# Kernel tuning notes

Measured on AMD Instinct MI355X. Metric: run time of the kernel, lower is better.

## Reference

```python
import jax, jax.numpy as jnp
import numpy as np

L, H, C, HS, E, K, V, BS = 2, 12, 768, 64, 8, 2, 32000, 1024
B, T = 2, 1024


def layer_norm(x, s, b):
    mu = x.mean(-1, keepdims=True)
    var = ((x - mu) ** 2).mean(-1, keepdims=True)
    return (x - mu) / jnp.sqrt(var + 1e-5) * s + b


def setup_inputs() -> dict:
    key = jax.random.key(0)
    ks = jax.random.split(key, 16)
    def n(k, shape, s=0.02):
        return jax.random.normal(k, shape, dtype=jnp.float32) * s
    return {
        'idx': jax.random.randint(ks[0], (B, T), 0, V),
        'targets': jax.random.randint(ks[1], (B, T), 0, V),
        'tok_emb': n(ks[2], (V, C)),
        'pos_emb': n(ks[3], (BS, C)),
        'ln1_s': jnp.ones((L, C), jnp.float32), 'ln1_b': jnp.zeros((L, C), jnp.float32),
        'wq': n(ks[4], (L, H, C, HS)), 'wk': n(ks[5], (L, H, C, HS)), 'wv': n(ks[6], (L, H, C, HS)),
        'wo': n(ks[7], (L, C, C)), 'bo': jnp.zeros((L, C), jnp.float32),
        'ln2_s': jnp.ones((L, C), jnp.float32), 'ln2_b': jnp.zeros((L, C), jnp.float32),
        'gate_w': n(ks[8], (L, E, C)),
        'w1': n(ks[9], (L, E, 4 * C, C)), 'b1': jnp.zeros((L, E, 4 * C), jnp.float32),
        'w2': n(ks[10], (L, E, C, 4 * C)), 'b2': jnp.zeros((L, E, C), jnp.float32),
        'lm_w': n(ks[11], (V, C)), 'lm_b': jnp.zeros((V,), jnp.float32),
    }


def reference(idx, targets, tok_emb, pos_emb, ln1_s, ln1_b, wq, wk, wv, wo, bo,
              ln2_s, ln2_b, gate_w, w1, b1, w2, b2, lm_w, lm_b):
    Bsz, Tn = idx.shape
    x = tok_emb[idx] + pos_emb[:Tn]                       # [B,T,C]
    mask = jnp.tril(jnp.ones((Tn, Tn), bool))
    for l in range(L):
        # causal multi-head attention (per-head projections, scale = n_embed**-0.5 as in source)
        h = layer_norm(x, ln1_s[l], ln1_b[l])
        q = jnp.einsum('btc,hcd->bhtd', h, wq[l])
        k = jnp.einsum('btc,hcd->bhtd', h, wk[l])
        v = jnp.einsum('btc,hcd->bhtd', h, wv[l])
        att = jnp.einsum('bhtd,bhsd->bhts', q, k) * (C ** -0.5)
        att = jax.nn.softmax(jnp.where(mask, att, -jnp.inf), axis=-1)
        o = jnp.einsum('bhts,bhsd->bhtd', att, v)
        o = o.transpose(0, 2, 1, 3).reshape(Bsz, Tn, C)   # concat heads
        x = x + jnp.einsum('btc,oc->bto', o, wo[l]) + bo[l]
        # MoE FFN: top-k routing, softmax over selected gate logits
        h2 = layer_norm(x, ln2_s[l], ln2_b[l]).reshape(-1, C)     # [N,C]
        gl = jnp.einsum('tc,ec->te', h2, gate_w[l])               # [N,E]
        wts, sel = jax.lax.top_k(gl, K)
        wts = jax.nn.softmax(wts, axis=-1)
        comb = jnp.einsum('tk,tke->te', wts, jax.nn.one_hot(sel, E, dtype=wts.dtype))
        hid = jax.nn.relu(jnp.einsum('tc,efc->etf', h2, w1[l]) + b1[l][:, None, :])
        y = jnp.einsum('etf,ecf->etc', hid, w2[l]) + b2[l][:, None, :]
        moe = jnp.einsum('te,etc->tc', comb, y)                   # dispatch-weighted combine
        x = x + moe.reshape(Bsz, Tn, C)
    logits = jnp.einsum('btc,vc->btv', x, lm_w) + lm_b
    lf = logits.reshape(-1, V)
    tf = targets.reshape(-1)
    loss = -jnp.take_along_axis(jax.nn.log_softmax(lf, axis=-1), tf[:, None], axis=1).mean()
    return lf, loss
```

## Files before the change

### kernel.cpp

```cpp
#include <hip/hip_runtime.h>
#include <hip/hip_bf16.h>

#define LCNT 2
#define HCNT 12
#define CDIM 768
#define HSD  64
#define ECNT 8
#define VOC  32000
#define BB   2
#define TT   1024
#define NTOK 2048
#define FF   3072
#define QKVLD 2304
#define TOTCAP 5120
#define SKN  4

typedef __attribute__((ext_vector_type(8))) short bf16x8;
typedef __attribute__((ext_vector_type(4))) float f32x4;

__device__ __forceinline__ float wave_sum(float v) {
    #pragma unroll
    for (int off = 32; off; off >>= 1) v += __shfl_xor(v, off);
    return v;
}
__device__ __forceinline__ float wave_max(float v) {
    #pragma unroll
    for (int off = 32; off; off >>= 1) v = fmaxf(v, __shfl_xor(v, off));
    return v;
}
__device__ __forceinline__ unsigned short f2bf(float f) {
    unsigned int u = __float_as_uint(f);
    unsigned int r = (u + 0x7FFFu + ((u >> 16) & 1u)) >> 16;
    return (unsigned short)r;
}
__device__ __forceinline__ float bf2f(unsigned short h) {
    return __uint_as_float((unsigned int)h << 16);
}
__device__ __forceinline__ void split2(float a, unsigned short& h, unsigned short& l) {
    h = f2bf(a);
    l = f2bf(a - bf2f(h));
}
__device__ __forceinline__ ushort4 cvt4(float4 v) {
    ushort4 r;
    r.x = f2bf(v.x); r.y = f2bf(v.y); r.z = f2bf(v.z); r.w = f2bf(v.w);
    return r;
}
__device__ __forceinline__ void gload16(const void* g, void* l) {
    __builtin_amdgcn_global_load_lds(
        (const __attribute__((address_space(1))) unsigned int*)g,
        (__attribute__((address_space(3))) unsigned int*)l,
        16, 0, 0);
}

__global__ __launch_bounds__(256)
void cvt_bf16_kernel(const float* __restrict__ in, unsigned short* __restrict__ out, int n4)
{
    for (int i = blockIdx.x * 256 + threadIdx.x; i < n4; i += gridDim.x * 256) {
        float4 v = reinterpret_cast<const float4*>(in)[i];
        reinterpret_cast<ushort4*>(out)[i] = cvt4(v);
    }
}

__global__ __launch_bounds__(256)
void splitw_kernel(const float* __restrict__ in, unsigned short* __restrict__ oh,
                   unsigned short* __restrict__ ol, int n4)
{
    for (int i = blockIdx.x * 256 + threadIdx.x; i < n4; i += gridDim.x * 256) {
        float4 v = reinterpret_cast<const float4*>(in)[i];
        ushort4 h, l;
        split2(v.x, h.x, l.x); split2(v.y, h.y, l.y);
        split2(v.z, h.z, l.z); split2(v.w, h.w, l.w);
        reinterpret_cast<ushort4*>(oh)[i] = h;
        reinterpret_cast<ushort4*>(ol)[i] = l;
    }
}

__global__ __launch_bounds__(256)
void embed_kernel(const int* __restrict__ idx, const float* __restrict__ tok,
                  const float* __restrict__ pos, float* __restrict__ x)
{
    int i = blockIdx.x * 256 + threadIdx.x;
    int c = i % CDIM;
    int n = i / CDIM;
    int t = n % TT;
    x[i] = tok[(size_t)idx[n] * CDIM + c] + pos[(size_t)t * CDIM + c];
}

__global__ __launch_bounds__(256)
void repack_kernel(const float* __restrict__ wq, const float* __restrict__ wk,
                   const float* __restrict__ wv, unsigned short* __restrict__ wph,
                   unsigned short* __restrict__ wpl)
{
    int i = blockIdx.x * 256 + threadIdx.x;
    int kk = i % CDIM;
    int n  = (i / CDIM) % CDIM;
    int w3 = (i / (CDIM * CDIM)) % 3;
    int l  = i / (CDIM * CDIM * 3);
    const float* src = (w3 == 0) ? wq : (w3 == 1) ? wk : wv;
    int h = n / HSD, d = n % HSD;
    float v = src[((((size_t)l * HCNT + h) * CDIM) + kk) * HSD + d];
    unsigned short hh, ll;
    split2(v, hh, ll);
    size_t o = (((size_t)l * 3 + w3) * CDIM + n) * CDIM + kk;
    wph[o] = hh;
    wpl[o] = ll;
}

template<bool WF32>
__global__ __launch_bounds__(256)
void ln_kernel(const float* __restrict__ x, const float* __restrict__ sc,
               const float* __restrict__ bs, float* __restrict__ out,
               unsigned short* __restrict__ oh, unsigned short* __restrict__ ol)
{
    int row = blockIdx.x;
    const float* xr = x + (size_t)row * CDIM;
    int tid = threadIdx.x;
    float v0 = xr[tid], v1 = xr[tid + 256], v2 = xr[tid + 512];
    float s1 = v0 + v1 + v2;
    float s2 = v0 * v0 + v1 * v1 + v2 * v2;
    s1 = wave_sum(s1);
    s2 = wave_sum(s2);
    __shared__ float r1[4], r2[4];
    int w = tid >> 6, lane = tid & 63;
    if (lane == 0) { r1[w] = s1; r2[w] = s2; }
    __syncthreads();
    float t1 = r1[0] + r1[1] + r1[2] + r1[3];
    float t2 = r2[0] + r2[1] + r2[2] + r2[3];
    float mu = t1 * (1.0f / CDIM);
    float var = t2 * (1.0f / CDIM) - mu * mu;
    float rstd = rsqrtf(var + 1e-5f);
    float o0 = (v0 - mu) * rstd * sc[tid]       + bs[tid];
    float o1 = (v1 - mu) * rstd * sc[tid + 256] + bs[tid + 256];
    float o2 = (v2 - mu) * rstd * sc[tid + 512] + bs[tid + 512];
    if constexpr (WF32) {
        float* orow = out + (size_t)row * CDIM;
        orow[tid] = o0; orow[tid + 256] = o1; orow[tid + 512] = o2;
    }
    unsigned short h, l;
    unsigned short* ohr = oh + (size_t)row * CDIM;
    unsigned short* olr = ol + (size_t)row * CDIM;
    split2(o0, h, l); ohr[tid]       = h; olr[tid]       = l;
    split2(o1, h, l); ohr[tid + 256] = h; olr[tid + 256] = l;
    split2(o2, h, l); ohr[tid + 512] = h; olr[tid + 512] = l;
}

#define BM 128
#define BN 128
#define BK 32
#define PADK 40

template<int MODE, bool OUTSPLIT>
__global__ __launch_bounds__(256)
void gemm_ps_kernel(int Kd,
                    const unsigned short* __restrict__ Ahg,
                    const unsigned short* __restrict__ Alg, int lda,
                    const unsigned short* __restrict__ Bhg,
                    const unsigned short* __restrict__ Blg, int ldb,
                    const float* __restrict__ bias,
                    float* __restrict__ out,
                    unsigned short* __restrict__ outh,
                    unsigned short* __restrict__ outl, int ldo)
{
    __shared__ short Ah[BM * PADK];
    __shared__ short Al[BM * PADK];
    __shared__ short Bh[BN * PADK];
    __shared__ short Bl[BN * PADK];

    const int tid = threadIdx.x;
    const int m0 = blockIdx.y * BM;
    const int n0 = blockIdx.x * BN;
    const int w = tid >> 6, lane = tid & 63;
    const int wr = w >> 1, wc = w & 1;
    const int lrow = lane & 15, lkg = lane >> 4;
    const int srow = tid >> 3, skg = (tid & 7) * 4;

    const unsigned short* Ahb = Ahg + (size_t)m0 * lda;
    const unsigned short* Alb = Alg + (size_t)m0 * lda;
    const unsigned short* Bhb = Bhg + (size_t)n0 * ldb;
    const unsigned short* Blb = Blg + (size_t)n0 * ldb;

    ushort4 pah[4], pal[4], pbh[4], pbl[4];
    #pragma unroll
    for (int p = 0; p < 4; ++p) {
        pah[p] = *(const ushort4*)(Ahb + (size_t)(p * 32 + srow) * lda + skg);
        pal[p] = *(const ushort4*)(Alb + (size_t)(p * 32 + srow) * lda + skg);
        pbh[p] = *(const ushort4*)(Bhb + (size_t)(p * 32 + srow) * ldb + skg);
        pbl[p] = *(const ushort4*)(Blb + (size_t)(p * 32 + srow) * ldb + skg);
    }

    f32x4 acc[4][4] = {};
    const int nk = Kd / BK;

    for (int t = 0; t < nk; ++t) {
        __syncthreads();
        #pragma unroll
        for (int p = 0; p < 4; ++p) {
            *(ushort4*)(&Ah[(p * 32 + srow) * PADK + skg]) = pah[p];
            *(ushort4*)(&Al[(p * 32 + srow) * PADK + skg]) = pal[p];
            *(ushort4*)(&Bh[(p * 32 + srow) * PADK + skg]) = pbh[p];
            *(ushort4*)(&Bl[(p * 32 + srow) * PADK + skg]) = pbl[p];
        }
        __syncthreads();
        if (t + 1 < nk) {
            const int kb = (t + 1) * BK + skg;
            #pragma unroll
            for (int p = 0; p < 4; ++p) {
                pah[p] = *(const ushort4*)(Ahb + (size_t)(p * 32 + srow) * lda + kb);
                pal[p] = *(const ushort4*)(Alb + (size_t)(p * 32 + srow) * lda + kb);
                pbh[p] = *(const ushort4*)(Bhb + (size_t)(p * 32 + srow) * ldb + kb);
                pbl[p] = *(const ushort4*)(Blb + (size_t)(p * 32 + srow) * ldb + kb);
            }
        }
        bf16x8 afh[4], afl[4];
        #pragma unroll
        for (int i = 0; i < 4; ++i) {
            afh[i] = *(const bf16x8*)(&Ah[(wr * 64 + i * 16 + lrow) * PADK + lkg * 8]);
            afl[i] = *(const bf16x8*)(&Al[(wr * 64 + i * 16 + lrow) * PADK + lkg * 8]);
        }
        #pragma unroll
        for (int j = 0; j < 4; ++j) {
            const bf16x8 bh = *(const bf16x8*)(&Bh[(wc * 64 + j * 16 + lrow) * PADK + lkg * 8]);
            const bf16x8 bl = *(const bf16x8*)(&Bl[(wc * 64 + j * 16 + lrow) * PADK + lkg * 8]);
            #pragma unroll
            for (int i = 0; i < 4; ++i) {
                acc[i][j] = __builtin_amdgcn_mfma_f32_16x16x32_bf16(afh[i], bh, acc[i][j], 0, 0, 0);
                acc[i][j] = __builtin_amdgcn_mfma_f32_16x16x32_bf16(afl[i], bh, acc[i][j], 0, 0, 0);
                acc[i][j] = __builtin_amdgcn_mfma_f32_16x16x32_bf16(afh[i], bl, acc[i][j], 0, 0, 0);
            }
        }
    }

    #pragma unroll
    for (int i = 0; i < 4; ++i) {
        #pragma unroll
        for (int r = 0; r < 4; ++r) {
            const int row = m0 + wr * 64 + i * 16 + lkg * 4 + r;
            #pragma unroll
            for (int j = 0; j < 4; ++j) {
                const int col = n0 + wc * 64 + j * 16 + lrow;
                const float bj = bias ? bias[col] : 0.0f;
                const float vres = acc[i][j][r] + bj;
                if constexpr (OUTSPLIT) {
                    unsigned short h, l;
                    split2(vres, h, l);
                    outh[(size_t)row * ldo + col] = h;
                    outl[(size_t)row * ldo + col] = l;
                } else {
                    float* op = out + (size_t)row * ldo + col;
                    if (MODE == 0) *op = vres;
                    else *op = *op + vres;
                }
            }
        }
    }
}

__global__ __launch_bounds__(256)
void gemm_pse_kernel(int Kd,
                     const unsigned short* __restrict__ Ahg,
                     const unsigned short* __restrict__ Alg, int lda,
                     const float* __restrict__ B, int ldb,
                     const float* __restrict__ bias,
                     unsigned short* __restrict__ outh,
                     unsigned short* __restrict__ outl, int ldo,
                     const int* __restrict__ rowmeta,
                     size_t bstride, int biasstride)
{
    __shared__ short Ah[BM * PADK];
    __shared__ short Al[BM * PADK];
    __shared__ short Bh[BN * PADK];
    __shared__ short Bl[BN * PADK];

    const int ee = blockIdx.z;
    const int rcnt = rowmeta[2 * ee + 1];
    if ((int)(blockIdx.y * BM) >= rcnt) return;
    const int roff = rowmeta[2 * ee];
    B += (size_t)ee * bstride;
    bias += (size_t)ee * biasstride;

    const int tid = threadIdx.x;
    const int m0 = roff + blockIdx.y * BM;
    const int n0 = blockIdx.x * BN;
    const int w = tid >> 6, lane = tid & 63;
    const int wr = w >> 1, wc = w & 1;
    const int lrow = lane & 15, lkg = lane >> 4;
    const int srow = tid >> 3, skg = (tid & 7) * 4;

    const unsigned short* Ahb = Ahg + (size_t)m0 * lda;
    const unsigned short* Alb = Alg + (size_t)m0 * lda;
    const float* Bblk = B + (size_t)n0 * ldb;

    ushort4 pah[4], pal[4];
    float4 pb[4];
    #pragma unroll
    for (int p = 0; p < 4; ++p) {
        pah[p] = *(const ushort4*)(Ahb + (size_t)(p * 32 + srow) * lda + skg);
        pal[p] = *(const ushort4*)(Alb + (size_t)(p * 32 + srow) * lda + skg);
        pb[p]  = *(const float4*)(Bblk + (size_t)(p * 32 + srow) * ldb + skg);
    }

    f32x4 acc[4][4] = {};
    const int nk = Kd / BK;

    for (int t = 0; t < nk; ++t) {
        __syncthreads();
        #pragma unroll
        for (int p = 0; p < 4; ++p) {
            *(ushort4*)(&Ah[(p * 32 + srow) * PADK + skg]) = pah[p];
            *(ushort4*)(&Al[(p * 32 + srow) * PADK + skg]) = pal[p];
            ushort4 h, l;
            split2(pb[p].x, h.x, l.x); split2(pb[p].y, h.y, l.y);
            split2(pb[p].z, h.z, l.z); split2(pb[p].w, h.w, l.w);
            *(ushort4*)(&Bh[(p * 32 + srow) * PADK + skg]) = h;
            *(ushort4*)(&Bl[(p * 32 + srow) * PADK + skg]) = l;
        }
        __syncthreads();
        if (t + 1 < nk) {
            const int kb = (t + 1) * BK + skg;
            #pragma unroll
            for (int p = 0; p < 4; ++p) {
                pah[p] = *(const ushort4*)(Ahb + (size_t)(p * 32 + srow) * lda + kb);
                pal[p] = *(const ushort4*)(Alb + (size_t)(p * 32 + srow) * lda + kb);
                pb[p]  = *(const float4*)(Bblk + (size_t)(p * 32 + srow) * ldb + kb);
            }
        }
        bf16x8 afh[4], afl[4];
        #pragma unroll
        for (int i = 0; i < 4; ++i) {
            afh[i] = *(const bf16x8*)(&Ah[(wr * 64 + i * 16 + lrow) * PADK + lkg * 8]);
            afl[i] = *(const bf16x8*)(&Al[(wr * 64 + i * 16 + lrow) * PADK + lkg * 8]);
        }
        #pragma unroll
        for (int j = 0; j < 4; ++j) {
            const bf16x8 bh = *(const bf16x8*)(&Bh[(wc * 64 + j * 16 + lrow) * PADK + lkg * 8]);
            const bf16x8 bl = *(const bf16x8*)(&Bl[(wc * 64 + j * 16 + lrow) * PADK + lkg * 8]);
            #pragma unroll
            for (int i = 0; i < 4; ++i) {
                acc[i][j] = __builtin_amdgcn_mfma_f32_16x16x32_bf16(afh[i], bh, acc[i][j], 0, 0, 0);
                acc[i][j] = __builtin_amdgcn_mfma_f32_16x16x32_bf16(afl[i], bh, acc[i][j], 0, 0, 0);
                acc[i][j] = __builtin_amdgcn_mfma_f32_16x16x32_bf16(afh[i], bl, acc[i][j], 0, 0, 0);
            }
        }
    }

    #pragma unroll
    for (int i = 0; i < 4; ++i) {
        #pragma unroll
        for (int r = 0; r < 4; ++r) {
            const int row = m0 + wr * 64 + i * 16 + lkg * 4 + r;
            #pragma unroll
            for (int j = 0; j < 4; ++j) {
                const int col = n0 + wc * 64 + j * 16 + lrow;
                const float vres = fmaxf(acc[i][j][r] + bias[col], 0.0f);
                unsigned short h, l;
                split2(vres, h, l);
                outh[(size_t)row * ldo + col] = h;
                outl[(size_t)row * ldo + col] = l;
            }
        }
    }
}

template<int SK>
__global__ __launch_bounds__(256)
void gemm_pssk_kernel(int Kc,
                      const unsigned short* __restrict__ Ahg,
                      const unsigned short* __restrict__ Alg, int lda,
                      const float* __restrict__ B, int ldb,
                      const float* __restrict__ bias,
                      float* __restrict__ part, int ldo, size_t pstride,
                      const int* __restrict__ rowmeta,
                      size_t bstride, int biasstride)
{
    __shared__ short Ah[BM * PADK];
    __shared__ short Al[BM * PADK];
    __shared__ short Bh[BN * PADK];
    __shared__ short Bl[BN * PADK];

    const int zz = blockIdx.z;
    const int ee = zz / SK, kz = zz % SK;
    const int rcnt = rowmeta[2 * ee + 1];
    if ((int)(blockIdx.y * BM) >= rcnt) return;
    const int roff = rowmeta[2 * ee];
    const float* Bp = B + (size_t)ee * bstride + (size_t)kz * Kc;
    const unsigned short* Ahp = Ahg + (size_t)kz * Kc;
    const unsigned short* Alp = Alg + (size_t)kz * Kc;
    const float* biasp = (kz == 0) ? bias + (size_t)ee * biasstride : nullptr;
    float* out = part + (size_t)kz * pstride;

    const int tid = threadIdx.x;
    const int m0 = roff + blockIdx.y * BM;
    const int n0 = blockIdx.x * BN;
    const int w = tid >> 6, lane = tid & 63;
    const int wr = w >> 1, wc = w & 1;
    const int lrow = lane & 15, lkg = lane >> 4;
    const int srow = tid >> 3, skg = (tid & 7) * 4;

    const unsigned short* Ahb = Ahp + (size_t)m0 * lda;
    const unsigned short* Alb = Alp + (size_t)m0 * lda;
    const float* Bblk = Bp + (size_t)n0 * ldb;

    ushort4 pah[4], pal[4];
    float4 pb[4];
    #pragma unroll
    for (int p = 0; p < 4; ++p) {
        pah[p] = *(const ushort4*)(Ahb + (size_t)(p * 32 + srow) * lda + skg);
        pal[p] = *(const ushort4*)(Alb + (size_t)(p * 32 + srow) * lda + skg);
        pb[p]  = *(const float4*)(Bblk + (size_t)(p * 32 + srow) * ldb + skg);
    }

    f32x4 acc[4][4] = {};
    const int nk = Kc / BK;

    for (int t = 0; t < nk; ++t) {
        __syncthreads();
        #pragma unroll
        for (int p = 0; p < 4; ++p) {
            *(ushort4*)(&Ah[(p * 32 + srow) * PADK + skg]) = pah[p];
            *(ushort4*)(&Al[(p * 32 + srow) * PADK + skg]) = pal[p];
            ushort4 h, l;
            split2(pb[p].x, h.x, l.x); split2(pb[p].y, h.y, l.y);
            split2(pb[p].z, h.z, l.z); split2(pb[p].w, h.w, l.w);
            *(ushort4*)(&Bh[(p * 32 + srow) * PADK + skg]) = h;
            *(ushort4*)(&Bl[(p * 32 + srow) * PADK + skg]) = l;
        }
        __syncthreads();
        if (t + 1 < nk) {
            const int kb = (t + 1) * BK + skg;
            #pragma unroll
            for (int p = 0; p < 4; ++p) {
                pah[p] = *(const ushort4*)(Ahb + (size_t)(p * 32 + srow) * lda + kb);
                pal[p] = *(const ushort4*)(Alb + (size_t)(p * 32 + srow) * lda + kb);
                pb[p]  = *(const float4*)(Bblk + (size_t)(p * 32 + srow) * ldb + kb);
            }
        }
        bf16x8 afh[4], afl[4];
        #pragma unroll
        for (int i = 0; i < 4; ++i) {
            afh[i] = *(const bf16x8*)(&Ah[(wr * 64 + i * 16 + lrow) * PADK + lkg * 8]);
            afl[i] = *(const bf16x8*)(&Al[(wr * 64 + i * 16 + lrow) * PADK + lkg * 8]);
        }
        #pragma unroll
        for (int j = 0; j < 4; ++j) {
            const bf16x8 bh = *(const bf16x8*)(&Bh[(wc * 64 + j * 16 + lrow) * PADK + lkg * 8]);
            const bf16x8 bl = *(const bf16x8*)(&Bl[(wc * 64 + j * 16 + lrow) * PADK + lkg * 8]);
            #pragma unroll
            for (int i = 0; i < 4; ++i) {
                acc[i][j] = __builtin_amdgcn_mfma_f32_16x16x32_bf16(afh[i], bh, acc[i][j], 0, 0, 0);
                acc[i][j] = __builtin_amdgcn_mfma_f32_16x16x32_bf16(afl[i], bh, acc[i][j], 0, 0, 0);
                acc[i][j] = __builtin_amdgcn_mfma_f32_16x16x32_bf16(afh[i], bl, acc[i][j], 0, 0, 0);
            }
        }
    }

    #pragma unroll
    for (int i = 0; i < 4; ++i) {
        #pragma unroll
        for (int r = 0; r < 4; ++r) {
            const int row = m0 + wr * 64 + i * 16 + lkg * 4 + r;
            #pragma unroll
            for (int j = 0; j < 4; ++j) {
                const int col = n0 + wc * 64 + j * 16 + lrow;
                const float bj = biasp ? biasp[col] : 0.0f;
                out[(size_t)row * ldo + col] = acc[i][j][r] + bj;
            }
        }
    }
}

template<int MODE, bool SWZ, bool OUTBF, bool BBF>
__global__ __launch_bounds__(256)
void gemm_fastw_kernel(int Kd,
                       const unsigned short* __restrict__ A, int lda,
                       const void* __restrict__ Bv, int ldb,
                       const float* __restrict__ bias,
                       void* __restrict__ outv, int ldo,
                       const int* __restrict__ rowmeta,
                       size_t bstride, int biasstride)
{
    __shared__ short Ah[BM * PADK];
    __shared__ short Bh[BN * PADK];

    int bx = blockIdx.x, by = blockIdx.y;
    if constexpr (SWZ) {
        const int nwg = gridDim.x * gridDim.y;
        const int chunk = nwg >> 3;
        const int flat = by * gridDim.x + bx;
        const int newid = (flat & 7) * chunk + (flat >> 3);
        by = newid % gridDim.y;
        bx = newid / gridDim.y;
    }

    const float* Bf = (const float*)Bv;
    const unsigned short* Bb = (const unsigned short*)Bv;
    float* outf = (float*)outv;
    unsigned short* outb = (unsigned short*)outv;

    int roff = 0;
    if (rowmeta) {
        const int ee = blockIdx.z;
        const int rcnt = rowmeta[2 * ee + 1];
        if ((int)(by * BM) >= rcnt) return;
        roff = rowmeta[2 * ee];
        if (BBF) Bb += (size_t)ee * bstride; else Bf += (size_t)ee * bstride;
        if (bias) bias += (size_t)ee * biasstride;
    }

    const int tid = threadIdx.x;
    const int m0 = roff + by * BM;
    const int n0 = bx * BN;
    const int w = tid >> 6, lane = tid & 63;
    const int wr = w >> 1, wc = w & 1;
    const int lrow = lane & 15, lkg = lane >> 4;
    const int srow = tid >> 3, skg = (tid & 7) * 4;

    const unsigned short* Ablk = A + (size_t)m0 * lda;
    const float* Bfblk = Bf + (size_t)n0 * ldb;
    const unsigned short* Bbblk = Bb + (size_t)n0 * ldb;

    ushort4 pa[4];
    ushort4 pbb[4];
    float4  pbf[4];
    #pragma unroll
    for (int p = 0; p < 4; ++p) {
        pa[p] = *(const ushort4*)(Ablk + (size_t)(p * 32 + srow) * lda + skg);
        if constexpr (BBF) pbb[p] = *(const ushort4*)(Bbblk + (size_t)(p * 32 + srow) * ldb + skg);
        else               pbf[p] = *(const float4*)(Bfblk + (size_t)(p * 32 + srow) * ldb + skg);
    }

    f32x4 acc[4][4] = {};
    const int nk = Kd / BK;

    for (int t = 0; t < nk; ++t) {
        __syncthreads();
        #pragma unroll
        for (int p = 0; p < 4; ++p) {
            *(ushort4*)(&Ah[(p * 32 + srow) * PADK + skg]) = pa[p];
            *(ushort4*)(&Bh[(p * 32 + srow) * PADK + skg]) = BBF ? pbb[p] : cvt4(pbf[p]);
        }
        __syncthreads();
        if (t + 1 < nk) {
            const int kb = (t + 1) * BK + skg;
            #pragma unroll
            for (int p = 0; p < 4; ++p) {
                pa[p] = *(const ushort4*)(Ablk + (size_t)(p * 32 + srow) * lda + kb);
                if constexpr (BBF) pbb[p] = *(const ushort4*)(Bbblk + (size_t)(p * 32 + srow) * ldb + kb);
                else               pbf[p] = *(const float4*)(Bfblk + (size_t)(p * 32 + srow) * ldb + kb);
            }
        }
        bf16x8 af[4];
        #pragma unroll
        for (int i = 0; i < 4; ++i)
            af[i] = *(const bf16x8*)(&Ah[(wr * 64 + i * 16 + lrow) * PADK + lkg * 8]);
        #pragma unroll
        for (int j = 0; j < 4; ++j) {
            const bf16x8 bh = *(const bf16x8*)(&Bh[(wc * 64 + j * 16 + lrow) * PADK + lkg * 8]);
            #pragma unroll
            for (int i = 0; i < 4; ++i)
                acc[i][j] = __builtin_amdgcn_mfma_f32_16x16x32_bf16(af[i], bh, acc[i][j], 0, 0, 0);
        }
    }

    #pragma unroll
    for (int i = 0; i < 4; ++i) {
        #pragma unroll
        for (int r = 0; r < 4; ++r) {
            const int row = m0 + wr * 64 + i * 16 + lkg * 4 + r;
            #pragma unroll
            for (int j = 0; j < 4; ++j) {
                const int col = n0 + wc * 64 + j * 16 + lrow;
                const float bj = bias ? bias[col] : 0.0f;
                float vres = acc[i][j][r] + bj;
                if (MODE == 2) vres = fmaxf(vres, 0.0f);
                if constexpr (OUTBF) outb[(size_t)row * ldo + col] = f2bf(vres);
                else                 outf[(size_t)row * ldo + col] = vres;
            }
        }
    }
}

template<bool SWZ>
__global__ __launch_bounds__(256)
void gemm_lds2_kernel(int Kd,
                      const unsigned short* __restrict__ A, int lda,
                      const unsigned short* __restrict__ B, int ldb,
                      const float* __restrict__ bias,
                      float* __restrict__ out, int ldo)
{
    __shared__ unsigned short Asl[2][BM * BK];
    __shared__ unsigned short Bsl[2][BN * BK];

    int bx = blockIdx.x, by = blockIdx.y;
    if constexpr (SWZ) {
        const int nwg = gridDim.x * gridDim.y;
        const int chunk = nwg >> 3;
        const int flat = by * gridDim.x + bx;
        const int newid = (flat & 7) * chunk + (flat >> 3);
        by = newid % gridDim.y;
        bx = newid / gridDim.y;
    }

    const int tid = threadIdx.x;
    const int m0 = by * BM;
    const int n0 = bx * BN;
    const int w = tid >> 6, lane = tid & 63;
    const int wr = w >> 1, wc = w & 1;
    const int lrow = lane & 15, lkg = lane >> 4;
    const int grow = lane >> 2, gcol = (lane & 3) * 8;

    const unsigned short* Ablk = A + (size_t)m0 * lda;
    const unsigned short* Bblk = B + (size_t)n0 * ldb;

    f32x4 acc[4][4] = {};
    const int nk = Kd / BK;

    #pragma unroll
    for (int j = 0; j < 2; ++j) {
        const int rbase = w * 32 + j * 16;
        gload16(Ablk + (size_t)(rbase + grow) * lda + gcol, &Asl[0][rbase * BK]);
        gload16(Bblk + (size_t)(rbase + grow) * ldb + gcol, &Bsl[0][rbase * BK]);
    }
    __syncthreads();

    int cur = 0;
    for (int t = 0; t < nk; ++t) {
        if (t + 1 < nk) {
            const int k0 = (t + 1) * BK;
            #pragma unroll
            for (int j = 0; j < 2; ++j) {
                const int rbase = w * 32 + j * 16;
                gload16(Ablk + (size_t)(rbase + grow) * lda + k0 + gcol, &Asl[cur ^ 1][rbase * BK]);
                gload16(Bblk + (size_t)(rbase + grow) * ldb + k0 + gcol, &Bsl[cur ^ 1][rbase * BK]);
            }
        }
        bf16x8 af[4];
        #pragma unroll
        for (int i = 0; i < 4; ++i)
            af[i] = *(const bf16x8*)(&Asl[cur][(wr * 64 + i * 16 + lrow) * BK + lkg * 8]);
        #pragma unroll
        for (int j = 0; j < 4; ++j) {
            const bf16x8 bh = *(const bf16x8*)(&Bsl[cur][(wc * 64 + j * 16 + lrow) * BK + lkg * 8]);
            #pragma unroll
            for (int i = 0; i < 4; ++i)
                acc[i][j] = __builtin_amdgcn_mfma_f32_16x16x32_bf16(af[i], bh, acc[i][j], 0, 0, 0);
        }
        __syncthreads();
        cur ^= 1;
    }

    #pragma unroll
    for (int i = 0; i < 4; ++i) {
        #pragma unroll
        for (int r = 0; r < 4; ++r) {
            const int row = m0 + wr * 64 + i * 16 + lkg * 4 + r;
            #pragma unroll
            for (int j = 0; j < 4; ++j) {
                const int col = n0 + wc * 64 + j * 16 + lrow;
                const float bj = bias ? bias[col] : 0.0f;
                out[(size_t)row * ldo + col] = acc[i][j][r] + bj;
            }
        }
    }
}

#define QBLK 64
#define KVBLK 64

__global__ __launch_bounds__(256)
void attn_mfma_kernel(const unsigned short* __restrict__ qh_g,
                      const unsigned short* __restrict__ ql_g,
                      unsigned short* __restrict__ oh_g,
                      unsigned short* __restrict__ ol_g)
{
    __shared__ short Kh[2][KVBLK][PADK];
    __shared__ short Kl[2][KVBLK][PADK];
    __shared__ short Vh[2][HSD][PADK];
    __shared__ short Vl[2][HSD][PADK];
    __shared__ short Ph[4][2][16][PADK];
    __shared__ short Pl[4][2][16][PADK];

    const int t0 = blockIdx.x * QBLK;
    const int bh = blockIdx.y;
    const int b = bh / HCNT, hh = bh % HCNT;
    const size_t baseq = (size_t)b * TT * QKVLD + (size_t)hh * HSD;
    const size_t obase = (size_t)b * TT * CDIM + (size_t)hh * HSD;
    const unsigned short* kh_g = qh_g + baseq + CDIM;
    const unsigned short* kl_g = ql_g + baseq + CDIM;
    const unsigned short* vh_g = qh_g + baseq + 2 * CDIM;
    const unsigned short* vl_g = ql_g + baseq + 2 * CDIM;
    const int tid = threadIdx.x;
    const int w = tid >> 6, lane = tid & 63;
    const int lrow = lane & 15, lkg = lane >> 4;
    const float sscale = rsqrtf((float)CDIM);

    bf16x8 qh[2], ql[2];
    {
        const size_t qroff = baseq + (size_t)(t0 + w * 16 + lrow) * QKVLD;
        #pragma unroll
        for (int ks = 0; ks < 2; ++ks) {
            qh[ks] = *(const bf16x8*)(qh_g + qroff + ks * 32 + lkg * 8);
            ql[ks] = *(const bf16x8*)(ql_g + qroff + ks * 32 + lkg * 8);
        }
    }

    f32x4 oacc[4] = {};
    float m_[4], l_[4];
    #pragma unroll
    for (int rr = 0; rr < 4; ++rr) { m_[rr] = -1e30f; l_[rr] = 0.0f; }

    for (int s0 = 0; s0 <= t0 + QBLK - 1; s0 += KVBLK) {
        __syncthreads();
        {
            const int srow = tid >> 3, skg = (tid & 7) * 4;
            #pragma unroll
            for (int p = 0; p < 2; ++p) {
                const size_t kroff = (size_t)(s0 + p * 32 + srow) * QKVLD;
                #pragma unroll
                for (int ks = 0; ks < 2; ++ks) {
                    *(ushort4*)(&Kh[ks][p * 32 + srow][skg]) = *(const ushort4*)(kh_g + kroff + ks * 32 + skg);
                    *(ushort4*)(&Kl[ks][p * 32 + srow][skg]) = *(const ushort4*)(kl_g + kroff + ks * 32 + skg);
                }
            }
            const int key = tid & 63, dg = (tid >> 6) * 16;
            const size_t vroff = (size_t)(s0 + key) * QKVLD + dg;
            const int kst = key >> 5, ko = key & 31;
            #pragma unroll
            for (int dd = 0; dd < 16; dd += 4) {
                ushort4 hv = *(const ushort4*)(vh_g + vroff + dd);
                ushort4 lv = *(const ushort4*)(vl_g + vroff + dd);
                Vh[kst][dg + dd + 0][ko] = hv.x; Vl[kst][dg + dd + 0][ko] = lv.x;
                Vh[kst][dg + dd + 1][ko] = hv.y; Vl[kst][dg + dd + 1][ko] = lv.y;
                Vh[kst][dg + dd + 2][ko] = hv.z; Vl[kst][dg + dd + 2][ko] = lv.z;
                Vh[kst][dg + dd + 3][ko] = hv.w; Vl[kst][dg + dd + 3][ko] = lv.w;
            }
        }
        __syncthreads();

        f32x4 sacc[4] = {};
        #pragma unroll
        for (int j = 0; j < 4; ++j) {
            #pragma unroll
            for (int ks = 0; ks < 2; ++ks) {
                const bf16x8 bh = *(const bf16x8*)(&Kh[ks][j * 16 + lrow][lkg * 8]);
                const bf16x8 bl = *(const bf16x8*)(&Kl[ks][j * 16 + lrow][lkg * 8]);
                sacc[j] = __builtin_amdgcn_mfma_f32_16x16x32_bf16(qh[ks], bh, sacc[j], 0, 0, 0);
                sacc[j] = __builtin_amdgcn_mfma_f32_16x16x32_bf16(ql[ks], bh, sacc[j], 0, 0, 0);
                sacc[j] = __builtin_amdgcn_mfma_f32_16x16x32_bf16(qh[ks], bl, sacc[j], 0, 0, 0);
            }
        }

        #pragma unroll
        for (int rr = 0; rr < 4; ++rr) {
            const int qi = t0 + w * 16 + lkg * 4 + rr;
            float pv[4];
            float mx = -1e30f;
            #pragma unroll
            for (int j = 0; j < 4; ++j) {
                float s = sacc[j][rr] * sscale;
                if (s0 + j * 16 + lrow > qi) s = -1e30f;
                pv[j] = s;
                mx = fmaxf(mx, s);
            }
            #pragma unroll
            for (int off = 1; off < 16; off <<= 1) mx = fmaxf(mx, __shfl_xor(mx, off));
            const float mnew = fmaxf(m_[rr], mx);
            const float corr = __expf(m_[rr] - mnew);
            float ps = 0.0f;
            #pragma unroll
            for (int j = 0; j < 4; ++j) { pv[j] = __expf(pv[j] - mnew); ps += pv[j]; }
            #pragma unroll
            for (int off = 1; off < 16; off <<= 1) ps += __shfl_xor(ps, off);
            l_[rr] = l_[rr] * corr + ps;
            m_[rr] = mnew;
            #pragma unroll
            for (int jd = 0; jd < 4; ++jd) oacc[jd][rr] *= corr;
            #pragma unroll
            for (int j = 0; j < 4; ++j) {
                unsigned short h, l;
                split2(pv[j], h, l);
                const int key = j * 16 + lrow;
                Ph[w][key >> 5][lkg * 4 + rr][key & 31] = h;
                Pl[w][key >> 5][lkg * 4 + rr][key & 31] = l;
            }
        }

        #pragma unroll
        for (int ks = 0; ks < 2; ++ks) {
            const bf16x8 ah = *(const bf16x8*)(&Ph[w][ks][lrow][lkg * 8]);
            const bf16x8 al = *(const bf16x8*)(&Pl[w][ks][lrow][lkg * 8]);
            #pragma unroll
            for (int jd = 0; jd < 4; ++jd) {
                const bf16x8 bh = *(const bf16x8*)(&Vh[ks][jd * 16 + lrow][lkg * 8]);
                const bf16x8 bl = *(const bf16x8*)(&Vl[ks][jd * 16 + lrow][lkg * 8]);
                oacc[jd] = __builtin_amdgcn_mfma_f32_16x16x32_bf16(ah, bh, oacc[jd], 0, 0, 0);
                oacc[jd] = __builtin_amdgcn_mfma_f32_16x16x32_bf16(al, bh, oacc[jd], 0, 0, 0);
                oacc[jd] = __builtin_amdgcn_mfma_f32_16x16x32_bf16(ah, bl, oacc[jd], 0, 0, 0);
            }
        }
    }

    #pragma unroll
    for (int rr = 0; rr < 4; ++rr) {
        const int qi = t0 + w * 16 + lkg * 4 + rr;
        const float invl = 1.0f / l_[rr];
        const size_t orow = obase + (size_t)qi * CDIM;
        #pragma unroll
        for (int jd = 0; jd < 4; ++jd) {
            unsigned short h, l;
            split2(oacc[jd][rr] * invl, h, l);
            oh_g[orow + jd * 16 + lrow] = h;
            ol_g[orow + jd * 16 + lrow] = l;
        }
    }
}

__global__ __launch_bounds__(256)
void gate_kernel(const float* __restrict__ h2, const float* __restrict__ gw,
                 int2* __restrict__ sel, float2* __restrict__ wts)
{
    __shared__ float gws[ECNT * CDIM];
    int tid = threadIdx.x;
    for (int i = tid; i < ECNT * CDIM; i += 256) gws[i] = gw[i];
    __syncthreads();
    int t = blockIdx.x * 256 + tid;
    const float* hr = h2 + (size_t)t * CDIM;
    float g[ECNT] = {};
    for (int c = 0; c < CDIM; ++c) {
        float hv = hr[c];
        #pragma unroll
        for (int e = 0; e < ECNT; ++e) g[e] = fmaf(hv, gws[e * CDIM + c], g[e]);
    }
    int e0 = 0; float g0 = g[0];
    #pragma unroll
    for (int e = 1; e < ECNT; ++e) if (g[e] > g0) { g0 = g[e]; e0 = e; }
    int e1 = -1; float g1 = -1e30f;
    #pragma unroll
    for (int e = 0; e < ECNT; ++e) if (e != e0 && g[e] > g1) { g1 = g[e]; e1 = e; }
    float z = __expf(g1 - g0);
    float w0 = 1.0f / (1.0f + z);
    sel[t] = make_int2(e0, e1);
    wts[t] = make_float2(w0, 1.0f - w0);
}

__global__ __launch_bounds__(256)
void route_kernel(const int2* __restrict__ sel, int* __restrict__ perm,
                  int* __restrict__ tokpos, int* __restrict__ meta)
{
    __shared__ int cnt[ECNT], off[ECNT], cur[ECNT];
    const int tid = threadIdx.x;
    if (tid < ECNT) cnt[tid] = 0;
    __syncthreads();
    for (int t = tid; t < NTOK; t += 256) {
        atomicAdd(&cnt[sel[t].x], 1);
        atomicAdd(&cnt[sel[t].y], 1);
    }
    __syncthreads();
    if (tid == 0) {
        int run = 0;
        for (int e = 0; e < ECNT; ++e) {
            off[e] = run; cur[e] = 0;
            int pc = (cnt[e] + BM - 1) / BM * BM;
            meta[2 * e] = run; meta[2 * e + 1] = pc;
            run += pc;
        }
    }
    __syncthreads();
    for (int p = tid; p < TOTCAP; p += 256) perm[p] = 0;
    __syncthreads();
    for (int t = tid; t < NTOK; t += 256) {
        int2 s = sel[t];
        int p0 = atomicAdd(&cur[s.x], 1); perm[off[s.x] + p0] = t; tokpos[2 * t]     = off[s.x] + p0;
        int p1 = atomicAdd(&cur[s.y], 1); perm[off[s.y] + p1] = t; tokpos[2 * t + 1] = off[s.y] + p1;
    }
}

__global__ __launch_bounds__(256)
void gather_ps_kernel(const unsigned short* __restrict__ h2h,
                      const unsigned short* __restrict__ h2l,
                      const int* __restrict__ perm,
                      unsigned short* __restrict__ xgh,
                      unsigned short* __restrict__ xgl)
{
    int i = blockIdx.x * 256 + threadIdx.x;
    int c = i % CDIM, p = i / CDIM;
    const size_t s = (size_t)perm[p] * CDIM + c;
    xgh[i] = h2h[s];
    xgl[i] = h2l[s];
}

__global__ __launch_bounds__(256)
void gather_cp_kernel(const unsigned short* __restrict__ h2h, const int* __restrict__ perm,
                      unsigned short* __restrict__ xg)
{
    int i = blockIdx.x * 256 + threadIdx.x;
    int c = i % CDIM, p = i / CDIM;
    xg[i] = h2h[(size_t)perm[p] * CDIM + c];
}

template<int SK>
__global__ __launch_bounds__(256)
void combine_kernel(const float* __restrict__ y, size_t pstride,
                    const int* __restrict__ tokpos,
                    const float2* __restrict__ wts, float* __restrict__ x)
{
    int i = blockIdx.x * 256 + threadIdx.x;
    int c = i % CDIM, t = i / CDIM;
    float2 wv = wts[t];
    const size_t r0 = (size_t)tokpos[2 * t] * CDIM + c;
    const size_t r1 = (size_t)tokpos[2 * t + 1] * CDIM + c;
    float a0 = 0.0f, a1 = 0.0f;
    #pragma unroll
    for (int s = 0; s < SK; ++s) {
        a0 += y[s * pstride + r0];
        a1 += y[s * pstride + r1];
    }
    x[i] += wv.x * a0 + wv.y * a1;
}

__global__ __launch_bounds__(256)
void loss_row_kernel(const float* __restrict__ logits, const int* __restrict__ tgt,
                     float* __restrict__ lrow)
{
    int row = blockIdx.x;
    const float4* lr4 = (const float4*)(logits + (size_t)row * VOC);
    int tid = threadIdx.x, w = tid >> 6, lane = tid & 63;
    __shared__ float red[4];
    float mx = -1e30f;
    for (int i = tid; i < VOC / 4; i += 256) {
        float4 v = lr4[i];
        mx = fmaxf(mx, fmaxf(fmaxf(v.x, v.y), fmaxf(v.z, v.w)));
    }
    mx = wave_max(mx);
    if (lane == 0) red[w] = mx;
    __syncthreads();
    mx = fmaxf(fmaxf(red[0], red[1]), fmaxf(red[2], red[3]));
    __syncthreads();
    float se = 0.0f;
    for (int i = tid; i < VOC / 4; i += 256) {
        float4 v = lr4[i];
        se += expf(v.x - mx) + expf(v.y - mx) + expf(v.z - mx) + expf(v.w - mx);
    }
    se = wave_sum(se);
    if (lane == 0) red[w] = se;
    __syncthreads();
    if (tid == 0) {
        float lse = mx + logf(red[0] + red[1] + red[2] + red[3]);
        lrow[row] = lse - logits[(size_t)row * VOC + tgt[row]];
    }
}

__global__ __launch_bounds__(256)
void loss_reduce_kernel(const float* __restrict__ lrow, float* __restrict__ out)
{
    int tid = threadIdx.x, w = tid >> 6, lane = tid & 63;
    float s = 0.0f;
    for (int i = tid; i < NTOK; i += 256) s += lrow[i];
    s = wave_sum(s);
    __shared__ float red[4];
    if (lane == 0) red[w] = s;
    __syncthreads();
    if (tid == 0) out[0] = (red[0] + red[1] + red[2] + red[3]) * (1.0f / NTOK);
}

extern "C" void kernel_launch(void* const* d_in, const int* in_sizes, int n_in,
                              void* d_out, int out_size, void* d_ws, size_t ws_size,
                              hipStream_t stream)
{
    const int*   idx     = (const int*)d_in[0];
    const int*   targets = (const int*)d_in[1];
    const float* tok_emb = (const float*)d_in[2];
    const float* pos_emb = (const float*)d_in[3];
    const float* ln1_s   = (const float*)d_in[4];
    const float* ln1_b   = (const float*)d_in[5];
    const float* wq      = (const float*)d_in[6];
    const float* wk      = (const float*)d_in[7];
    const float* wv      = (const float*)d_in[8];
    const float* wo      = (const float*)d_in[9];
    const float* bo      = (const float*)d_in[10];
    const float* ln2_s   = (const float*)d_in[11];
    const float* ln2_b   = (const float*)d_in[12];
    const float* gate_w  = (const float*)d_in[13];
    const float* w1      = (const float*)d_in[14];
    const float* b1      = (const float*)d_in[15];
    const float* w2      = (const float*)d_in[16];
    const float* b2      = (const float*)d_in[17];
    const float* lm_w    = (const float*)d_in[18];
    const float* lm_b    = (const float*)d_in[19];
    float* out = (float*)d_out;

    unsigned short* wph = (unsigned short*)d_ws;
    unsigned short* wpl = wph + (size_t)3 * LCNT * CDIM * CDIM;
    unsigned short* woh = wpl + (size_t)3 * LCNT * CDIM * CDIM;
    unsigned short* wol = woh + (size_t)LCNT * CDIM * CDIM;
    float* x    = (float*)(wol + (size_t)LCNT * CDIM * CDIM);
    float* hbuf = x    + (size_t)NTOK * CDIM;
    float* qkv  = hbuf + (size_t)NTOK * CDIM;
    float* xg   = qkv  + (size_t)NTOK * QKVLD;
    float* hid  = xg   + (size_t)TOTCAP * CDIM;
    float* lrow = hid  + (size_t)TOTCAP * FF;
    float2* wts = (float2*)(lrow + NTOK);
    int2*  sel  = (int2*)(wts + NTOK);
    int*   perm = (int*)(sel + NTOK);
    int*  tokpos= perm + TOTCAP;
    int*   meta = tokpos + 2 * NTOK;
    unsigned short* x_bf = (unsigned short*)(meta + 16);
    float* part = (float*)(x_bf + (size_t)NTOK * CDIM);

    const size_t need_bytes = (size_t)((char*)(part + (size_t)SKN * TOTCAP * CDIM) - (char*)d_ws);
    const bool use_sk = ws_size >= need_bytes;

    unsigned short* hbufh = (unsigned short*)hbuf;
    unsigned short* hbufl = hbufh + (size_t)NTOK * CDIM;
    unsigned short* qkvh = (unsigned short*)qkv;
    unsigned short* qkvl = qkvh + (size_t)NTOK * QKVLD;
    float*          h2   = qkv;
    unsigned short* h2h  = (unsigned short*)(qkv + (size_t)NTOK * CDIM);
    unsigned short* h2l  = h2h + (size_t)NTOK * CDIM;
    float*          ybuf = qkv;
    unsigned short* xgh  = (unsigned short*)xg;
    unsigned short* xgl  = xgh + (size_t)TOTCAP * CDIM;
    unsigned short* xg_bf = (unsigned short*)xg;
    unsigned short* hidh = (unsigned short*)hid;
    unsigned short* hidl = hidh + (size_t)TOTCAP * FF;
    unsigned short* hid_bf = (unsigned short*)hid;
    unsigned short* lmw_bf = (unsigned short*)hid;

    dim3 blk(256);

    repack_kernel<<<(3 * LCNT * CDIM * CDIM) / 256, blk, 0, stream>>>(wq, wk, wv, wph, wpl);
    splitw_kernel<<<1024, blk, 0, stream>>>(wo, woh, wol, LCNT * CDIM * CDIM / 4);
    embed_kernel<<<(NTOK * CDIM) / 256, blk, 0, stream>>>(idx, tok_emb, pos_emb, x);

    for (int l = 0; l < LCNT; ++l) {
        ln_kernel<false><<<NTOK, blk, 0, stream>>>(
            x, ln1_s + (size_t)l * CDIM, ln1_b + (size_t)l * CDIM, nullptr, hbufh, hbufl);

        gemm_ps_kernel<0, true><<<dim3(QKVLD / BN, NTOK / BM), blk, 0, stream>>>(
            CDIM, hbufh, hbufl, CDIM,
            wph + (size_t)l * 3 * CDIM * CDIM, wpl + (size_t)l * 3 * CDIM * CDIM, CDIM,
            nullptr, nullptr, qkvh, qkvl, QKVLD);

        attn_mfma_kernel<<<dim3(TT / QBLK, BB * HCNT), blk, 0, stream>>>(qkvh, qkvl, hbufh, hbufl);

        gemm_ps_kernel<1, false><<<dim3(CDIM / BN, NTOK / BM), blk, 0, stream>>>(
            CDIM, hbufh, hbufl, CDIM,
            woh + (size_t)l * CDIM * CDIM, wol + (size_t)l * CDIM * CDIM, CDIM,
            bo + (size_t)l * CDIM, x, nullptr, nullptr, CDIM);

        ln_kernel<true><<<NTOK, blk, 0, stream>>>(
            x, ln2_s + (size_t)l * CDIM, ln2_b + (size_t)l * CDIM, h2, h2h, h2l);
        gate_kernel<<<NTOK / 256, blk, 0, stream>>>(h2, gate_w + (size_t)l * ECNT * CDIM, sel, wts);
        route_kernel<<<1, blk, 0, stream>>>(sel, perm, tokpos, meta);

        const float* w1l = w1 + (size_t)l * ECNT * FF * CDIM;
        const float* b1l = b1 + (size_t)l * ECNT * FF;
        const float* w2l = w2 + (size_t)l * ECNT * CDIM * FF;
        const float* b2l = b2 + (size_t)l * ECNT * CDIM;
        if (l == 0) {
            gather_ps_kernel<<<(TOTCAP * CDIM) / 256, blk, 0, stream>>>(h2h, h2l, perm, xgh, xgl);
            gemm_pse_kernel<<<dim3(FF / BN, TOTCAP / BM, ECNT), blk, 0, stream>>>(
                CDIM, xgh, xgl, CDIM, w1l, CDIM, b1l, hidh, hidl, FF,
                meta, (size_t)FF * CDIM, FF);
            if (use_sk) {
                gemm_pssk_kernel<SKN><<<dim3(CDIM / BN, TOTCAP / BM, ECNT * SKN), blk, 0, stream>>>(
                    FF / SKN, hidh, hidl, FF, w2l, FF, b2l, part, CDIM, (size_t)TOTCAP * CDIM,
                    meta, (size_t)CDIM * FF, CDIM);
                combine_kernel<SKN><<<(NTOK * CDIM) / 256, blk, 0, stream>>>(
                    part, (size_t)TOTCAP * CDIM, tokpos, wts, x);
            } else {
                gemm_pssk_kernel<1><<<dim3(CDIM / BN, TOTCAP / BM, ECNT), blk, 0, stream>>>(
                    FF, hidh, hidl, FF, w2l, FF, b2l, ybuf, CDIM, 0,
                    meta, (size_t)CDIM * FF, CDIM);
                combine_kernel<1><<<(NTOK * CDIM) / 256, blk, 0, stream>>>(
                    ybuf, 0, tokpos, wts, x);
            }
        } else {
            gather_cp_kernel<<<(TOTCAP * CDIM) / 256, blk, 0, stream>>>(h2h, perm, xg_bf);
            gemm_fastw_kernel<2, false, true, false><<<dim3(FF / BN, TOTCAP / BM, ECNT), blk, 0, stream>>>(
                CDIM, xg_bf, CDIM, w1l, CDIM, b1l, hid_bf, FF, meta, (size_t)FF * CDIM, FF);
            gemm_fastw_kernel<0, false, false, false><<<dim3(CDIM / BN, TOTCAP / BM, ECNT), blk, 0, stream>>>(
                FF, hid_bf, FF, w2l, FF, b2l, ybuf, CDIM, meta, (size_t)CDIM * FF, CDIM);
            combine_kernel<1><<<(NTOK * CDIM) / 256, blk, 0, stream>>>(
                ybuf, 0, tokpos, wts, x);
        }
    }

    cvt_bf16_kernel<<<2048, blk, 0, stream>>>(lm_w, lmw_bf, VOC * CDIM / 4);
    cvt_bf16_kernel<<<512, blk, 0, stream>>>(x, x_bf, NTOK * CDIM / 4);

    gemm_lds2_kernel<true><<<dim3(VOC / BN, NTOK / BM), blk, 0, stream>>>(
        CDIM, x_bf, CDIM, lmw_bf, CDIM, lm_b, out, VOC);

    loss_row_kernel<<<NTOK, blk, 0, stream>>>(out, targets, lrow);
    loss_reduce_kernel<<<1, blk, 0, stream>>>(lrow, out + (size_t)NTOK * VOC);
}
```

Baseline: 1.319 ms.

## Fuse log-softmax partials into LM-head GEMM epilogue, swizzle LDS, emit bf16 x in combine

The LM-head GEMM epilogue now computes per-tile row max and sum-exp partials and writes them to workspace. A small final kernel merges these partials instead of re-reading the full 2048x32000 logits matrix twice. The GEMM's LDS layout gets an XOR swizzle to reduce bank conflicts. The last combine kernel writes the bf16 copy of x directly, which removes a separate conversion pass. Costs are extra epilogue shuffles and expf calls, plus a dependence on workspace size for the fused path.

Measured after the change: 1.362 ms. +3.3%, slower.

```diff
diff --git a/kernel.cpp b/kernel.cpp
--- a/kernel.cpp
+++ b/kernel.cpp
@@ -14,6 +14,7 @@
 #define QKVLD 2304
 #define TOTCAP 5120
 #define SKN  4
+#define NBLK (VOC / 128)
 
 typedef __attribute__((ext_vector_type(8))) short bf16x8;
 typedef __attribute__((ext_vector_type(4))) float f32x4;
@@ -579,16 +580,19 @@
     }
 }
 
-template<bool SWZ>
+template<bool SWZ, bool LOSSP>
 __global__ __launch_bounds__(256)
 void gemm_lds2_kernel(int Kd,
                       const unsigned short* __restrict__ A, int lda,
                       const unsigned short* __restrict__ B, int ldb,
                       const float* __restrict__ bias,
-                      float* __restrict__ out, int ldo)
+                      float* __restrict__ out, int ldo,
+                      float* __restrict__ maxp, float* __restrict__ sump)
 {
     __shared__ unsigned short Asl[2][BM * BK];
     __shared__ unsigned short Bsl[2][BN * BK];
+    __shared__ float redm[BM][2];
+    __shared__ float reds[BM][2];
 
     int bx = blockIdx.x, by = blockIdx.y;
     if constexpr (SWZ) {
@@ -606,7 +610,9 @@
     const int w = tid >> 6, lane = tid & 63;
     const int wr = w >> 1, wc = w & 1;
     const int lrow = lane & 15, lkg = lane >> 4;
-    const int grow = lane >> 2, gcol = (lane & 3) * 8;
+    const int grow = lane >> 2;
+    const int gcolS = (((lane & 3) ^ ((grow >> 1) & 3)) * 8);
+    const int rsw = (lkg ^ ((lrow >> 1) & 3)) * 8;
 
     const unsigned short* Ablk = A + (size_t)m0 * lda;
     const unsigned short* Bblk = B + (size_t)n0 * ldb;
@@ -617,8 +623,8 @@
     #pragma unroll
     for (int j = 0; j < 2; ++j) {
         const int rbase = w * 32 + j * 16;
-        gload16(Ablk + (size_t)(rbase + grow) * lda + gcol, &Asl[0][rbase * BK]);
-        gload16(Bblk + (size_t)(rbase + grow) * ldb + gcol, &Bsl[0][rbase * BK]);
+        gload16(Ablk + (size_t)(rbase + grow) * lda + gcolS, &Asl[0][rbase * BK]);
+        gload16(Bblk + (size_t)(rbase + grow) * ldb + gcolS, &Bsl[0][rbase * BK]);
     }
     __syncthreads();
 
@@ -629,17 +635,17 @@
             #pragma unroll
             for (int j = 0; j < 2; ++j) {
                 const int rbase = w * 32 + j * 16;
-                gload16(Ablk + (size_t)(rbase + grow) * lda + k0 + gcol, &Asl[cur ^ 1][rbase * BK]);
-                gload16(Bblk + (size_t)(rbase + grow) * ldb + k0 + gcol, &Bsl[cur ^ 1][rbase * BK]);
+                gload16(Ablk + (size_t)(rbase + grow) * lda + k0 + gcolS, &Asl[cur ^ 1][rbase * BK]);
+                gload16(Bblk + (size_t)(rbase + grow) * ldb + k0 + gcolS, &Bsl[cur ^ 1][rbase * BK]);
             }
         }
         bf16x8 af[4];
         #pragma unroll
         for (int i = 0; i < 4; ++i)
-            af[i] = *(const bf16x8*)(&Asl[cur][(wr * 64 + i * 16 + lrow) * BK + lkg * 8]);
+            af[i] = *(const bf16x8*)(&Asl[cur][(wr * 64 + i * 16 + lrow) * BK + rsw]);
         #pragma unroll
         for (int j = 0; j < 4; ++j) {
-            const bf16x8 bh = *(const bf16x8*)(&Bsl[cur][(wc * 64 + j * 16 + lrow) * BK + lkg * 8]);
+            const bf16x8 bh = *(const bf16x8*)(&Bsl[cur][(wc * 64 + j * 16 + lrow) * BK + rsw]);
             #pragma unroll
             for (int i = 0; i < 4; ++i)
                 acc[i][j] = __builtin_amdgcn_mfma_f32_16x16x32_bf16(af[i], bh, acc[i][j], 0, 0, 0);
@@ -653,12 +659,40 @@
         #pragma unroll
         for (int r = 0; r < 4; ++r) {
             const int row = m0 + wr * 64 + i * 16 + lkg * 4 + r;
+            float vj[4];
+            float mrow = -1e30f;
             #pragma unroll
             for (int j = 0; j < 4; ++j) {
                 const int col = n0 + wc * 64 + j * 16 + lrow;
                 const float bj = bias ? bias[col] : 0.0f;
-                out[(size_t)row * ldo + col] = acc[i][j][r] + bj;
-            }
+                vj[j] = acc[i][j][r] + bj;
+                out[(size_t)row * ldo + col] = vj[j];
+                mrow = fmaxf(mrow, vj[j]);
+            }
+            if constexpr (LOSSP) {
+                #pragma unroll
+                for (int off = 1; off < 16; off <<= 1) mrow = fmaxf(mrow, __shfl_xor(mrow, off));
+                float srow = 0.0f;
+                #pragma unroll
+                for (int j = 0; j < 4; ++j) srow += expf(vj[j] - mrow);
+                #pragma unroll
+                for (int off = 1; off < 16; off <<= 1) srow += __shfl_xor(srow, off);
+                if ((lane & 15) == 0) {
+                    const int lr_ = wr * 64 + i * 16 + lkg * 4 + r;
+                    redm[lr_][wc] = mrow;
+                    reds[lr_][wc] = srow;
+                }
+            }
+        }
+    }
+    if constexpr (LOSSP) {
+        __syncthreads();
+        if (tid < BM) {
+            const float ma = redm[tid][0], mb = redm[tid][1];
+            const float gm = fmaxf(ma, mb);
+            const float gs = reds[tid][0] * expf(ma - gm) + reds[tid][1] * expf(mb - gm);
+            maxp[(size_t)bx * NTOK + m0 + tid] = gm;
+            sump[(size_t)bx * NTOK + m0 + tid] = gs;
         }
     }
 }
@@ -897,11 +931,12 @@
     xg[i] = h2h[(size_t)perm[p] * CDIM + c];
 }
 
-template<int SK>
+template<int SK, bool EMITBF>
 __global__ __launch_bounds__(256)
 void combine_kernel(const float* __restrict__ y, size_t pstride,
                     const int* __restrict__ tokpos,
-                    const float2* __restrict__ wts, float* __restrict__ x)
+                    const float2* __restrict__ wts, float* __restrict__ x,
+                    unsigned short* __restrict__ xbf)
 {
     int i = blockIdx.x * 256 + threadIdx.x;
     int c = i % CDIM, t = i / CDIM;
@@ -914,7 +949,9 @@
         a0 += y[s * pstride + r0];
         a1 += y[s * pstride + r1];
     }
-    x[i] += wv.x * a0 + wv.y * a1;
+    const float nx = x[i] + wv.x * a0 + wv.y * a1;
+    x[i] = nx;
+    if constexpr (EMITBF) xbf[i] = f2bf(nx);
 }
 
 __global__ __launch_bounds__(256)
@@ -947,6 +984,21 @@
         float lse = mx + logf(red[0] + red[1] + red[2] + red[3]);
         lrow[row] = lse - logits[(size_t)row * VOC + tgt[row]];
     }
+}
+
+__global__ __launch_bounds__(256)
+void loss_final_kernel(const float* __restrict__ maxp, const float* __restrict__ sump,
+                       const float* __restrict__ logits, const int* __restrict__ tgt,
+                       float* __restrict__ lrow)
+{
+    int row = blockIdx.x * 256 + threadIdx.x;
+    float gm = -1e30f;
+    for (int i = 0; i < NBLK; ++i) gm = fmaxf(gm, maxp[(size_t)i * NTOK + row]);
+    float gs = 0.0f;
+    for (int i = 0; i < NBLK; ++i)
+        gs += sump[(size_t)i * NTOK + row] * expf(maxp[(size_t)i * NTOK + row] - gm);
+    const float lse = gm + logf(gs);
+    lrow[row] = lse - logits[(size_t)row * VOC + tgt[row]];
 }
 
 __global__ __launch_bounds__(256)
@@ -1005,9 +1057,13 @@
     int*   meta = tokpos + 2 * NTOK;
     unsigned short* x_bf = (unsigned short*)(meta + 16);
     float* part = (float*)(x_bf + (size_t)NTOK * CDIM);
-
-    const size_t need_bytes = (size_t)((char*)(part + (size_t)SKN * TOTCAP * CDIM) - (char*)d_ws);
-    const bool use_sk = ws_size >= need_bytes;
+    float* maxp = part + (size_t)SKN * TOTCAP * CDIM;
+    float* sump = maxp + (size_t)NBLK * NTOK;
+
+    const size_t need_sk    = (size_t)((char*)maxp - (char*)d_ws);
+    const size_t need_fused = (size_t)((char*)(sump + (size_t)NBLK * NTOK) - (char*)d_ws);
+    const bool use_sk     = ws_size >= need_sk;
+    const bool fused_loss = ws_size >= need_fused;
 
     unsigned short* hbufh = (unsigned short*)hbuf;
     unsigned short* hbufl = hbufh + (size_t)NTOK * CDIM;
@@ -1065,14 +1121,14 @@
                 gemm_pssk_kernel<SKN><<<dim3(CDIM / BN, TOTCAP / BM, ECNT * SKN), blk, 0, stream>>>(
                     FF / SKN, hidh, hidl, FF, w2l, FF, b2l, part, CDIM, (size_t)TOTCAP * CDIM,
                     meta, (size_t)CDIM * FF, CDIM);
-                combine_kernel<SKN><<<(NTOK * CDIM) / 256, blk, 0, stream>>>(
-                    part, (size_t)TOTCAP * CDIM, tokpos, wts, x);
+                combine_kernel<SKN, false><<<(NTOK * CDIM) / 256, blk, 0, stream>>>(
+                    part, (size_t)TOTCAP * CDIM, tokpos, wts, x, nullptr);
             } else {
                 gemm_pssk_kernel<1><<<dim3(CDIM / BN, TOTCAP / BM, ECNT), blk, 0, stream>>>(
                     FF, hidh, hidl, FF, w2l, FF, b2l, ybuf, CDIM, 0,
                     meta, (size_t)CDIM * FF, CDIM);
-                combine_kernel<1><<<(NTOK * CDIM) / 256, blk, 0, stream>>>(
-                    ybuf, 0, tokpos, wts, x);
+                combine_kernel<1, false><<<(NTOK * CDIM) / 256, blk, 0, stream>>>(
+                    ybuf, 0, tokpos, wts, x, nullptr);
             }
         } else {
             gather_cp_kernel<<<(TOTCAP * CDIM) / 256, blk, 0, stream>>>(h2h, perm, xg_bf);
@@ -1080,17 +1136,21 @@
                 CDIM, xg_bf, CDIM, w1l, CDIM, b1l, hid_bf, FF, meta, (size_t)FF * CDIM, FF);
             gemm_fastw_kernel<0, false, false, false><<<dim3(CDIM / BN, TOTCAP / BM, ECNT), blk, 0, stream>>>(
                 FF, hid_bf, FF, w2l, FF, b2l, ybuf, CDIM, meta, (size_t)CDIM * FF, CDIM);
-            combine_kernel<1><<<(NTOK * CDIM) / 256, blk, 0, stream>>>(
-                ybuf, 0, tokpos, wts, x);
+            combine_kernel<1, true><<<(NTOK * CDIM) / 256, blk, 0, stream>>>(
+                ybuf, 0, tokpos, wts, x, x_bf);
         }
     }
 
     cvt_bf16_kernel<<<2048, blk, 0, stream>>>(lm_w, lmw_bf, VOC * CDIM / 4);
-    cvt_bf16_kernel<<<512, blk, 0, stream>>>(x, x_bf, NTOK * CDIM / 4);
-
-    gemm_lds2_kernel<true><<<dim3(VOC / BN, NTOK / BM), blk, 0, stream>>>(
-        CDIM, x_bf, CDIM, lmw_bf, CDIM, lm_b, out, VOC);
-
-    loss_row_kernel<<<NTOK, blk, 0, stream>>>(out, targets, lrow);
+
+    if (fused_loss) {
+        gemm_lds2_kernel<true, true><<<dim3(VOC / BN, NTOK / BM), blk, 0, stream>>>(
+            CDIM, x_bf, CDIM, lmw_bf, CDIM, lm_b, out, VOC, maxp, sump);
+        loss_final_kernel<<<NTOK / 256, blk, 0, stream>>>(maxp, sump, out, targets, lrow);
+    } else {
+        gemm_lds2_kernel<true, false><<<dim3(VOC / BN, NTOK / BM), blk, 0, stream>>>(
+            CDIM, x_bf, CDIM, lmw_bf, CDIM, lm_b, out, VOC, nullptr, nullptr);
+        loss_row_kernel<<<NTOK, blk, 0, stream>>>(out, targets, lrow);
+    }
     loss_reduce_kernel<<<1, blk, 0, stream>>>(lrow, out + (size_t)NTOK * VOC);
 }
```
